# Optimization experiments

Measured on AMD Instinct MI355X. Metric: run time of the kernel, lower is better.

## Reference

```python
import jax, jax.numpy as jnp
import numpy as np

N_NODES = 100000
N_EDGES = 3200000
NFEAT = 256
NHID = 256
NCLASS = 64


def setup_inputs() -> dict:
    key = jax.random.key(0)
    ks = jax.random.split(key, 12)
    x = jax.random.normal(ks[0], (N_NODES, NFEAT), dtype=jnp.float32)
    edge_src = jax.random.randint(ks[1], (N_EDGES,), 0, N_NODES, dtype=jnp.int32)
    edge_dst = jnp.sort(jax.random.randint(ks[2], (N_EDGES,), 0, N_NODES, dtype=jnp.int32))
    edge_w = jax.random.uniform(ks[3], (N_EDGES,), dtype=jnp.float32)
    s1 = 1.0 / np.sqrt(NFEAT)
    s2 = 1.0 / np.sqrt(NHID)
    W1 = jax.random.normal(ks[4], (NFEAT, NHID), dtype=jnp.float32) * s1
    b1 = jnp.zeros((NHID,), dtype=jnp.float32)
    W2 = jax.random.normal(ks[5], (NHID, NHID), dtype=jnp.float32) * s2
    b2 = jnp.zeros((NHID,), dtype=jnp.float32)
    WL1 = jax.random.normal(ks[6], (NHID, NCLASS), dtype=jnp.float32) * s2
    bL1 = jnp.zeros((NCLASS,), dtype=jnp.float32)
    WL2 = jax.random.normal(ks[7], (NHID, NCLASS), dtype=jnp.float32) * s2
    bL2 = jnp.zeros((NCLASS,), dtype=jnp.float32)
    return {"x": x, "edge_src": edge_src, "edge_dst": edge_dst, "edge_w": edge_w,
            "W1": W1, "b1": b1, "W2": W2, "b2": b2,
            "WL1": WL1, "bL1": bL1, "WL2": WL2, "bL2": bL2}


def reference(x, edge_src, edge_dst, edge_w, W1, b1, W2, b2, WL1, bL1, WL2, bL2):
    n = x.shape[0]

    def spmm(h):
        # adj @ h with adj given as (src, dst, w) edge list:
        # out[dst] += w * h[src]
        return jax.ops.segment_sum(edge_w[:, None] * h[edge_src], edge_dst, num_segments=n)

    # GraphConvolution layer 1: support = x @ W; out = adj @ support + b; relu
    # (dropout inactive in eval mode)
    h = jax.nn.relu(spmm(x @ W1) + b1)
    # GraphConvolution layer 2
    h = jax.nn.relu(spmm(h @ W2) + b2)
    # twin dense heads
    logit1 = h @ WL1 + bL1
    logit2 = h @ WL2 + bL2
    return (logit1, logit2)
```

## Files before the change

kernel.cpp:

```cpp
#include <hip/hip_runtime.h>
#include <hip/hip_bf16.h>

typedef __attribute__((ext_vector_type(8))) short short8;
typedef __attribute__((ext_vector_type(4))) float f32x4;
typedef __attribute__((ext_vector_type(2))) float f32x2;

__device__ inline unsigned short f2bf(float f) {
    union { float f; unsigned int u; } x; x.f = f;
    return (unsigned short)((x.u + 0x7fffu + ((x.u >> 16) & 1u)) >> 16);
}

#define ASYNC16(gptr, lptr)                                                      \
    __builtin_amdgcn_global_load_lds(                                            \
        (const __attribute__((address_space(1))) unsigned int*)(gptr),           \
        (__attribute__((address_space(3))) unsigned int*)(lptr), 16, 0, 0)

__device__ __host__ inline int sg(int j) {
    int p = j & 63;
    return (j & ~63) | ((p >> 2) + 16 * (p & 3));
}

__global__ void rowptr_kernel(const int* __restrict__ dst, int* __restrict__ rp,
                              int E, int N) {
    int e = blockIdx.x * blockDim.x + threadIdx.x;
    if (e >= E) return;
    int d1 = dst[e];
    int d0 = (e == 0) ? -1 : dst[e - 1];
    for (int n = d0 + 1; n <= d1; n++) rp[n] = e;
    if (e <= N) {
        int dlast = dst[E - 1];
        if (e > dlast) rp[e] = E;
    }
}

__global__ void epack_kernel(const int* __restrict__ src, const float* __restrict__ w,
                             unsigned int* __restrict__ ep, int E4) {
    int i = blockIdx.x * blockDim.x + threadIdx.x;
    if (i >= E4) return;
    const int4 sv = ((const int4*)src)[i];
    const float4 wv = ((const float4*)w)[i];
    uint4 o;
    o.x = ((unsigned int)(f2bf(wv.x) & 0x7fffu) << 17) | (unsigned int)sv.x;
    o.y = ((unsigned int)(f2bf(wv.y) & 0x7fffu) << 17) | (unsigned int)sv.y;
    o.z = ((unsigned int)(f2bf(wv.z) & 0x7fffu) << 17) | (unsigned int)sv.z;
    o.w = ((unsigned int)(f2bf(wv.w) & 0x7fffu) << 17) | (unsigned int)sv.w;
    ((uint4*)ep)[i] = o;
}

__device__ inline float unpackw(unsigned int p) {
    return __uint_as_float((p >> 17) << 16);
}

__global__ void x2bf_kernel(const float* __restrict__ x, unsigned short* __restrict__ xb,
                            int n8) {
    int i = blockIdx.x * blockDim.x + threadIdx.x;
    if (i >= n8) return;
    const uint4* p = (const uint4*)(x + (size_t)i * 8);
    uint4 u = p[0], v = p[1];
    uint4 pk;
    pk.x = ((u.x + 0x8000u) >> 16) | ((u.y + 0x8000u) & 0xffff0000u);
    pk.y = ((u.z + 0x8000u) >> 16) | ((u.w + 0x8000u) & 0xffff0000u);
    pk.z = ((v.x + 0x8000u) >> 16) | ((v.y + 0x8000u) & 0xffff0000u);
    pk.w = ((v.z + 0x8000u) >> 16) | ((v.w + 0x8000u) & 0xffff0000u);
    *(uint4*)(xb + (size_t)i * 8) = pk;
}

__global__ void prep_kernel(const float* __restrict__ W1, const float* __restrict__ W2,
                            const float* __restrict__ WL1, const float* __restrict__ WL2,
                            const float* __restrict__ b1, const float* __restrict__ b2,
                            unsigned short* __restrict__ W1t, unsigned short* __restrict__ W2t,
                            unsigned short* __restrict__ WLt,
                            float* __restrict__ b1p, float* __restrict__ b2p) {
    int b = blockIdx.x, k = threadIdx.x;
    if (b < 256) {
        W1t[(size_t)b * 256 + k] = f2bf(W1[(size_t)k * 256 + b]);
    } else if (b < 512) {
        int n = b - 256;
        W2t[(size_t)n * 256 + k] = f2bf(W2[(size_t)sg(k) * 256 + n]);
    } else if (b < 640) {
        int c = b - 512;
        int ks = sg(k);
        float v = (c < 64) ? WL1[(size_t)ks * 64 + c] : WL2[(size_t)ks * 64 + (c - 64)];
        WLt[(size_t)c * 256 + k] = f2bf(v);
    } else if (b == 640) {
        b1p[k] = b1[sg(k)];
    } else {
        b2p[k] = b2[sg(k)];
    }
}

__global__ __launch_bounds__(256) void gemm_f8_kernel(
    const unsigned short* __restrict__ A, const unsigned short* __restrict__ Bt,
    unsigned char* __restrict__ C, int M)
{
    __shared__ __align__(16) unsigned short As[128 * 32];
    __shared__ __align__(16) unsigned short Bs[128 * 32];
    const int t = threadIdx.x;
    const int row0 = blockIdx.y * 128;
    const int col0 = blockIdx.x * 128;
    const int wid = t >> 6, lane = t & 63;
    const int wm = (wid >> 1) * 64, wn = (wid & 1) * 64;
    const int qk = (lane >> 4) * 8, r16 = lane & 15;

    const int c0 = t, c1 = t + 256;
    const int am0 = min(row0 + (c0 >> 2), M - 1);
    const int am1 = min(row0 + (c1 >> 2), M - 1);
    const int ak0 = (c0 & 3) * 8, ak1 = (c1 & 3) * 8;
    const int bm0 = col0 + (c0 >> 2), bm1 = col0 + (c1 >> 2);

    f32x4 acc[4][4];
#pragma unroll
    for (int i = 0; i < 4; i++)
#pragma unroll
        for (int j = 0; j < 4; j++) acc[i][j] = (f32x4){0.f, 0.f, 0.f, 0.f};

    for (int k0 = 0; k0 < 256; k0 += 32) {
        ASYNC16(A + (size_t)am0 * 256 + k0 + ak0, &As[c0 * 8]);
        ASYNC16(A + (size_t)am1 * 256 + k0 + ak1, &As[c1 * 8]);
        ASYNC16(Bt + (size_t)bm0 * 256 + k0 + ak0, &Bs[c0 * 8]);
        ASYNC16(Bt + (size_t)bm1 * 256 + k0 + ak1, &Bs[c1 * 8]);
        __syncthreads();
        short8 av[4], bv[4];
#pragma unroll
        for (int mt = 0; mt < 4; mt++) av[mt] = *(const short8*)(&As[(wm + mt * 16 + r16) * 32 + qk]);
#pragma unroll
        for (int nt = 0; nt < 4; nt++) bv[nt] = *(const short8*)(&Bs[(wn + nt * 16 + r16) * 32 + qk]);
#pragma unroll
        for (int mt = 0; mt < 4; mt++)
#pragma unroll
            for (int nt = 0; nt < 4; nt++)
                acc[mt][nt] = __builtin_amdgcn_mfma_f32_16x16x32_bf16(av[mt], bv[nt], acc[mt][nt], 0, 0, 0);
        __syncthreads();
    }
#pragma unroll
    for (int mt = 0; mt < 4; mt++) {
        const int rowb = row0 + wm + mt * 16 + (lane >> 4) * 4;
#pragma unroll
        for (int r = 0; r < 4; r++) {
            const int row = rowb + r;
            if (row >= M) continue;
            int w = 0;
            w = __builtin_amdgcn_cvt_pk_fp8_f32(acc[mt][0][r], acc[mt][1][r], w, false);
            w = __builtin_amdgcn_cvt_pk_fp8_f32(acc[mt][2][r], acc[mt][3][r], w, true);
            *(unsigned int*)(C + (size_t)row * 256 + col0 + wn + r16 * 4) = (unsigned int)w;
        }
    }
}

__global__ __launch_bounds__(256) void head_kernel(
    const unsigned short* __restrict__ A, const unsigned short* __restrict__ Bt,
    const float* __restrict__ bL1, const float* __restrict__ bL2,
    float* __restrict__ out, int M)
{
    __shared__ __align__(16) unsigned short As[128 * 32];
    __shared__ __align__(16) unsigned short Bs[128 * 32];
    const int t = threadIdx.x;
    const int row0 = blockIdx.x * 128;
    const int wid = t >> 6, lane = t & 63;
    const int wm = (wid >> 1) * 64, wn = (wid & 1) * 64;
    const int qk = (lane >> 4) * 8, r16 = lane & 15;

    const int c0 = t, c1 = t + 256;
    const int am0 = min(row0 + (c0 >> 2), M - 1);
    const int am1 = min(row0 + (c1 >> 2), M - 1);
    const int ak0 = (c0 & 3) * 8, ak1 = (c1 & 3) * 8;
    const int bm0 = c0 >> 2, bm1 = c1 >> 2;

    f32x4 acc[4][4];
#pragma unroll
    for (int i = 0; i < 4; i++)
#pragma unroll
        for (int j = 0; j < 4; j++) acc[i][j] = (f32x4){0.f, 0.f, 0.f, 0.f};

    for (int k0 = 0; k0 < 256; k0 += 32) {
        ASYNC16(A + (size_t)am0 * 256 + k0 + ak0, &As[c0 * 8]);
        ASYNC16(A + (size_t)am1 * 256 + k0 + ak1, &As[c1 * 8]);
        ASYNC16(Bt + (size_t)bm0 * 256 + k0 + ak0, &Bs[c0 * 8]);
        ASYNC16(Bt + (size_t)bm1 * 256 + k0 + ak1, &Bs[c1 * 8]);
        __syncthreads();
        short8 av[4], bv[4];
#pragma unroll
        for (int mt = 0; mt < 4; mt++) av[mt] = *(const short8*)(&As[(wm + mt * 16 + r16) * 32 + qk]);
#pragma unroll
        for (int nt = 0; nt < 4; nt++) bv[nt] = *(const short8*)(&Bs[(wn + nt * 16 + r16) * 32 + qk]);
#pragma unroll
        for (int mt = 0; mt < 4; mt++)
#pragma unroll
            for (int nt = 0; nt < 4; nt++)
                acc[mt][nt] = __builtin_amdgcn_mfma_f32_16x16x32_bf16(av[mt], bv[nt], acc[mt][nt], 0, 0, 0);
        __syncthreads();
    }
#pragma unroll
    for (int mt = 0; mt < 4; mt++) {
#pragma unroll
        for (int r = 0; r < 4; r++) {
            int row = row0 + wm + mt * 16 + (lane >> 4) * 4 + r;
            if (row >= M) continue;
#pragma unroll
            for (int nt = 0; nt < 4; nt++) {
                int col = wn + nt * 16 + r16;
                float v = acc[mt][nt][r];
                if (col < 64) {
                    out[(size_t)row * 64 + col] = v + bL1[col];
                } else {
                    out[(size_t)M * 64 + (size_t)row * 64 + (col - 64)] = v + bL2[col - 64];
                }
            }
        }
    }
}

__device__ inline void acc16f8(float* a, uint4 r, float w) {
    f32x2 p;
    p = __builtin_amdgcn_cvt_pk_f32_fp8((int)r.x, false); a[0]  += w * p.x; a[1]  += w * p.y;
    p = __builtin_amdgcn_cvt_pk_f32_fp8((int)r.x, true);  a[2]  += w * p.x; a[3]  += w * p.y;
    p = __builtin_amdgcn_cvt_pk_f32_fp8((int)r.y, false); a[4]  += w * p.x; a[5]  += w * p.y;
    p = __builtin_amdgcn_cvt_pk_f32_fp8((int)r.y, true);  a[6]  += w * p.x; a[7]  += w * p.y;
    p = __builtin_amdgcn_cvt_pk_f32_fp8((int)r.z, false); a[8]  += w * p.x; a[9]  += w * p.y;
    p = __builtin_amdgcn_cvt_pk_f32_fp8((int)r.z, true);  a[10] += w * p.x; a[11] += w * p.y;
    p = __builtin_amdgcn_cvt_pk_f32_fp8((int)r.w, false); a[12] += w * p.x; a[13] += w * p.y;
    p = __builtin_amdgcn_cvt_pk_f32_fp8((int)r.w, true);  a[14] += w * p.x; a[15] += w * p.y;
}

__global__ __launch_bounds__(256) void spmm_fp8_kernel(
    const unsigned char* __restrict__ sup, const int* __restrict__ rp,
    const unsigned int* __restrict__ ep, const float* __restrict__ bias,
    unsigned short* __restrict__ out, int nnodes)
{
    const int wid = threadIdx.x >> 6, lane = threadIdx.x & 63;
    const int node = blockIdx.x * 4 + wid;
    if (node >= nnodes) return;
    const int g = lane >> 4;
    const int f16 = (lane & 15) * 16;
    const unsigned char* supf = sup + f16;
    const int beg = rp[node], end = rp[node + 1];

    float a[16];
#pragma unroll
    for (int i = 0; i < 16; i++) a[i] = 0.f;

    int e = beg;
    const int nmain = (end - beg) >> 3;
    if (nmain > 0) {
        unsigned int cp0 = ep[e + g], cp1 = ep[e + 4 + g];
        uint4 cr0 = *(const uint4*)(supf + (size_t)(cp0 & 0x1ffffu) * 256);
        uint4 cr1 = *(const uint4*)(supf + (size_t)(cp1 & 0x1ffffu) * 256);
        unsigned int np0 = 0, np1 = 0;
        if (nmain > 1) {
            np0 = ep[e + 8 + g]; np1 = ep[e + 12 + g];
        }
        for (int it = 0; it + 1 < nmain; ++it) {
            const uint4 nr0 = *(const uint4*)(supf + (size_t)(np0 & 0x1ffffu) * 256);
            const uint4 nr1 = *(const uint4*)(supf + (size_t)(np1 & 0x1ffffu) * 256);
            unsigned int mp0 = 0, mp1 = 0;
            if (it + 2 < nmain) {
                const int eb = e + (it + 2) * 8;
                mp0 = ep[eb + g]; mp1 = ep[eb + 4 + g];
            }
            acc16f8(a, cr0, unpackw(cp0));
            acc16f8(a, cr1, unpackw(cp1));
            cr0 = nr0; cr1 = nr1; cp0 = np0; cp1 = np1;
            np0 = mp0; np1 = mp1;
        }
        acc16f8(a, cr0, unpackw(cp0));
        acc16f8(a, cr1, unpackw(cp1));
        e += nmain * 8;
    }
    for (; e + 4 <= end; e += 4) {
        const unsigned int p = ep[e + g];
        const uint4 r = *(const uint4*)(supf + (size_t)(p & 0x1ffffu) * 256);
        acc16f8(a, r, unpackw(p));
    }
    {
        const int rem = end - e;
        if (g < rem) {
            const unsigned int p = ep[e + g];
            const uint4 r = *(const uint4*)(supf + (size_t)(p & 0x1ffffu) * 256);
            acc16f8(a, r, unpackw(p));
        }
    }
#pragma unroll
    for (int i = 0; i < 16; i++) {
        a[i] += __shfl_xor(a[i], 16);
        a[i] += __shfl_xor(a[i], 32);
    }

    if (g == 0) {
        const float4 b0 = *(const float4*)(bias + f16);
        const float4 b1 = *(const float4*)(bias + f16 + 4);
        const float4 b2 = *(const float4*)(bias + f16 + 8);
        const float4 b3 = *(const float4*)(bias + f16 + 12);
        a[0] += b0.x; a[1] += b0.y; a[2]  += b0.z; a[3]  += b0.w;
        a[4] += b1.x; a[5] += b1.y; a[6]  += b1.z; a[7]  += b1.w;
        a[8] += b2.x; a[9] += b2.y; a[10] += b2.z; a[11] += b2.w;
        a[12] += b3.x; a[13] += b3.y; a[14] += b3.z; a[15] += b3.w;
#pragma unroll
        for (int i = 0; i < 16; i++) a[i] = a[i] > 0.f ? a[i] : 0.f;
        uint4 o0, o1;
        o0.x = (unsigned int)f2bf(a[0])  | ((unsigned int)f2bf(a[1])  << 16);
        o0.y = (unsigned int)f2bf(a[2])  | ((unsigned int)f2bf(a[3])  << 16);
        o0.z = (unsigned int)f2bf(a[4])  | ((unsigned int)f2bf(a[5])  << 16);
        o0.w = (unsigned int)f2bf(a[6])  | ((unsigned int)f2bf(a[7])  << 16);
        o1.x = (unsigned int)f2bf(a[8])  | ((unsigned int)f2bf(a[9])  << 16);
        o1.y = (unsigned int)f2bf(a[10]) | ((unsigned int)f2bf(a[11]) << 16);
        o1.z = (unsigned int)f2bf(a[12]) | ((unsigned int)f2bf(a[13]) << 16);
        o1.w = (unsigned int)f2bf(a[14]) | ((unsigned int)f2bf(a[15]) << 16);
        *(uint4*)(out + (size_t)node * 256 + f16) = o0;
        *(uint4*)(out + (size_t)node * 256 + f16 + 8) = o1;
    }
}

__global__ __launch_bounds__(256) void spmm_fp8_raw_kernel(
    const unsigned char* __restrict__ sup, const int* __restrict__ rp,
    const int* __restrict__ esrc, const float* __restrict__ ew,
    const float* __restrict__ bias, unsigned short* __restrict__ out, int nnodes)
{
    const int wid = threadIdx.x >> 6, lane = threadIdx.x & 63;
    const int node = blockIdx.x * 4 + wid;
    if (node >= nnodes) return;
    const int g = lane >> 4;
    const int f16 = (lane & 15) * 16;
    const unsigned char* supf = sup + f16;
    const int beg = rp[node], end = rp[node + 1];

    float a[16];
#pragma unroll
    for (int i = 0; i < 16; i++) a[i] = 0.f;

    int e = beg;
    for (; e + 8 <= end; e += 8) {
        const int s0 = esrc[e + g],     s1 = esrc[e + 4 + g];
        const float w0 = ew[e + g],     w1 = ew[e + 4 + g];
        const uint4 r0 = *(const uint4*)(supf + (size_t)s0 * 256);
        const uint4 r1 = *(const uint4*)(supf + (size_t)s1 * 256);
        acc16f8(a, r0, w0);
        acc16f8(a, r1, w1);
    }
    for (; e + 4 <= end; e += 4) {
        const int s = esrc[e + g];
        const float w = ew[e + g];
        const uint4 r = *(const uint4*)(supf + (size_t)s * 256);
        acc16f8(a, r, w);
    }
    {
        const int rem = end - e;
        if (g < rem) {
            const int s = esrc[e + g];
            const float w = ew[e + g];
            const uint4 r = *(const uint4*)(supf + (size_t)s * 256);
            acc16f8(a, r, w);
        }
    }
#pragma unroll
    for (int i = 0; i < 16; i++) {
        a[i] += __shfl_xor(a[i], 16);
        a[i] += __shfl_xor(a[i], 32);
    }

    if (g == 0) {
        const float4 b0 = *(const float4*)(bias + f16);
        const float4 b1 = *(const float4*)(bias + f16 + 4);
        const float4 b2 = *(const float4*)(bias + f16 + 8);
        const float4 b3 = *(const float4*)(bias + f16 + 12);
        a[0] += b0.x; a[1] += b0.y; a[2]  += b0.z; a[3]  += b0.w;
        a[4] += b1.x; a[5] += b1.y; a[6]  += b1.z; a[7]  += b1.w;
        a[8] += b2.x; a[9] += b2.y; a[10] += b2.z; a[11] += b2.w;
        a[12] += b3.x; a[13] += b3.y; a[14] += b3.z; a[15] += b3.w;
#pragma unroll
        for (int i = 0; i < 16; i++) a[i] = a[i] > 0.f ? a[i] : 0.f;
        uint4 o0, o1;
        o0.x = (unsigned int)f2bf(a[0])  | ((unsigned int)f2bf(a[1])  << 16);
        o0.y = (unsigned int)f2bf(a[2])  | ((unsigned int)f2bf(a[3])  << 16);
        o0.z = (unsigned int)f2bf(a[4])  | ((unsigned int)f2bf(a[5])  << 16);
        o0.w = (unsigned int)f2bf(a[6])  | ((unsigned int)f2bf(a[7])  << 16);
        o1.x = (unsigned int)f2bf(a[8])  | ((unsigned int)f2bf(a[9])  << 16);
        o1.y = (unsigned int)f2bf(a[10]) | ((unsigned int)f2bf(a[11]) << 16);
        o1.z = (unsigned int)f2bf(a[12]) | ((unsigned int)f2bf(a[13]) << 16);
        o1.w = (unsigned int)f2bf(a[14]) | ((unsigned int)f2bf(a[15]) << 16);
        *(uint4*)(out + (size_t)node * 256 + f16) = o0;
        *(uint4*)(out + (size_t)node * 256 + f16 + 8) = o1;
    }
}

extern "C" void kernel_launch(void* const* d_in, const int* in_sizes, int n_in,
                              void* d_out, int out_size, void* d_ws, size_t ws_size,
                              hipStream_t stream) {
    const float* x    = (const float*)d_in[0];
    const int*   esrc = (const int*)d_in[1];
    const int*   edst = (const int*)d_in[2];
    const float* ew   = (const float*)d_in[3];
    const float* W1   = (const float*)d_in[4];
    const float* b1   = (const float*)d_in[5];
    const float* W2   = (const float*)d_in[6];
    const float* b2   = (const float*)d_in[7];
    const float* WL1  = (const float*)d_in[8];
    const float* bL1  = (const float*)d_in[9];
    const float* WL2  = (const float*)d_in[10];
    const float* bL2  = (const float*)d_in[11];
    float* out = (float*)d_out;

    const int N = in_sizes[0] / 256;
    const int E = in_sizes[1];

    char* ws = (char*)d_ws;
    size_t off = 0;
    auto alloc = [&](size_t bytes) -> void* {
        void* p = ws + off;
        off = (off + bytes + 511) & ~(size_t)511;
        return p;
    };
    int* rp              = (int*)alloc((size_t)(N + 1) * 4);
    unsigned short* W1t  = (unsigned short*)alloc((size_t)256 * 256 * 2);
    unsigned short* W2t  = (unsigned short*)alloc((size_t)256 * 256 * 2);
    unsigned short* WLt  = (unsigned short*)alloc((size_t)128 * 256 * 2);
    float* b1p           = (float*)alloc(256 * 4);
    float* b2p           = (float*)alloc(256 * 4);
    unsigned char* sup8  = (unsigned char*)alloc((size_t)N * 256);
    unsigned short* hbuf = (unsigned short*)alloc((size_t)N * 256 * 2);
    unsigned int* ep     = (unsigned int*)alloc((size_t)E * 4);
    const bool packed = (off <= ws_size);

    const int mblocks = (N + 127) / 128;

    rowptr_kernel<<<(E + 255) / 256, 256, 0, stream>>>(edst, rp, E, N);
    if (packed)
        epack_kernel<<<(E / 4 + 255) / 256, 256, 0, stream>>>(esrc, ew, ep, E / 4);
    x2bf_kernel<<<(N * 256 / 8 + 255) / 256, 256, 0, stream>>>(x, hbuf, N * 256 / 8);
    prep_kernel<<<642, 256, 0, stream>>>(W1, W2, WL1, WL2, b1, b2, W1t, W2t, WLt, b1p, b2p);

    gemm_f8_kernel<<<dim3(2, mblocks), 256, 0, stream>>>(hbuf, W1t, sup8, N);
    if (packed)
        spmm_fp8_kernel<<<(N + 3) / 4, 256, 0, stream>>>(sup8, rp, ep, b1p, hbuf, N);
    else
        spmm_fp8_raw_kernel<<<(N + 3) / 4, 256, 0, stream>>>(sup8, rp, esrc, ew, b1p, hbuf, N);
    gemm_f8_kernel<<<dim3(2, mblocks), 256, 0, stream>>>(hbuf, W2t, sup8, N);
    if (packed)
        spmm_fp8_kernel<<<(N + 3) / 4, 256, 0, stream>>>(sup8, rp, ep, b2p, hbuf, N);
    else
        spmm_fp8_raw_kernel<<<(N + 3) / 4, 256, 0, stream>>>(sup8, rp, esrc, ew, b2p, hbuf, N);
    head_kernel<<<mblocks, 256, 0, stream>>>(hbuf, WLt, bL1, bL2, out, N);
}
```

Baseline: 506.2 us.

## Fuse fp32-to-bf16 input conversion into first GEMM and use packed FMA in SpMM

Drops the separate x-to-bf16 conversion kernel and has a new first-layer GEMM read the fp32 input directly, converting each tile to bf16 in registers before storing it to LDS. This removes one full write and re-read of a bf16 copy of x (about 50 MB of traffic) and one kernel launch. Separately, the SpMM accumulation switches to inline-asm v_pk_fma_f32 on float pairs to halve the FMA instruction count. The fused GEMM loads A synchronously instead of through async LDS copies, which may expose more load latency, and because x is fp32 each block reads twice as many A bytes as before.

```diff
diff --git a/kernel.cpp b/kernel.cpp
--- a/kernel.cpp
+++ b/kernel.cpp
@@ -49,20 +49,6 @@
 
 __device__ inline float unpackw(unsigned int p) {
     return __uint_as_float((p >> 17) << 16);
-}
-
-__global__ void x2bf_kernel(const float* __restrict__ x, unsigned short* __restrict__ xb,
-                            int n8) {
-    int i = blockIdx.x * blockDim.x + threadIdx.x;
-    if (i >= n8) return;
-    const uint4* p = (const uint4*)(x + (size_t)i * 8);
-    uint4 u = p[0], v = p[1];
-    uint4 pk;
-    pk.x = ((u.x + 0x8000u) >> 16) | ((u.y + 0x8000u) & 0xffff0000u);
-    pk.y = ((u.z + 0x8000u) >> 16) | ((u.w + 0x8000u) & 0xffff0000u);
-    pk.z = ((v.x + 0x8000u) >> 16) | ((v.y + 0x8000u) & 0xffff0000u);
-    pk.w = ((v.z + 0x8000u) >> 16) | ((v.w + 0x8000u) & 0xffff0000u);
-    *(uint4*)(xb + (size_t)i * 8) = pk;
 }
 
 __global__ void prep_kernel(const float* __restrict__ W1, const float* __restrict__ W2,
@@ -89,6 +75,78 @@
     }
 }
 
+__global__ __launch_bounds__(256) void gemm_f8_x32_kernel(
+    const float* __restrict__ A, const unsigned short* __restrict__ Bt,
+    unsigned char* __restrict__ C, int M)
+{
+    __shared__ __align__(16) unsigned short As[128 * 32];
+    __shared__ __align__(16) unsigned short Bs[128 * 32];
+    const int t = threadIdx.x;
+    const int row0 = blockIdx.y * 128;
+    const int col0 = blockIdx.x * 128;
+    const int wid = t >> 6, lane = t & 63;
+    const int wm = (wid >> 1) * 64, wn = (wid & 1) * 64;
+    const int qk = (lane >> 4) * 8, r16 = lane & 15;
+
+    const int c0 = t, c1 = t + 256;
+    const int am0 = min(row0 + (c0 >> 2), M - 1);
+    const int am1 = min(row0 + (c1 >> 2), M - 1);
+    const int ak0 = (c0 & 3) * 8, ak1 = (c1 & 3) * 8;
+    const int bm0 = col0 + (c0 >> 2), bm1 = col0 + (c1 >> 2);
+
+    f32x4 acc[4][4];
+#pragma unroll
+    for (int i = 0; i < 4; i++)
+#pragma unroll
+        for (int j = 0; j < 4; j++) acc[i][j] = (f32x4){0.f, 0.f, 0.f, 0.f};
+
+    for (int k0 = 0; k0 < 256; k0 += 32) {
+        ASYNC16(Bt + (size_t)bm0 * 256 + k0 + ak0, &Bs[c0 * 8]);
+        ASYNC16(Bt + (size_t)bm1 * 256 + k0 + ak1, &Bs[c1 * 8]);
+        const float* pa0 = A + (size_t)am0 * 256 + k0 + ak0;
+        const float* pa1 = A + (size_t)am1 * 256 + k0 + ak1;
+        const uint4 u0 = *(const uint4*)pa0, v0 = *(const uint4*)(pa0 + 4);
+        const uint4 u1 = *(const uint4*)pa1, v1 = *(const uint4*)(pa1 + 4);
+        uint4 pk0, pk1;
+        pk0.x = ((u0.x + 0x8000u) >> 16) | ((u0.y + 0x8000u) & 0xffff0000u);
+        pk0.y = ((u0.z + 0x8000u) >> 16) | ((u0.w + 0x8000u) & 0xffff0000u);
+        pk0.z = ((v0.x + 0x8000u) >> 16) | ((v0.y + 0x8000u) & 0xffff0000u);
+        pk0.w = ((v0.z + 0x8000u) >> 16) | ((v0.w + 0x8000u) & 0xffff0000u);
+        pk1.x = ((u1.x + 0x8000u) >> 16) | ((u1.y + 0x8000u) & 0xffff0000u);
+        pk1.y = ((u1.z + 0x8000u) >> 16) | ((u1.w + 0x8000u) & 0xffff0000u);
+        pk1.z = ((v1.x + 0x8000u) >> 16) | ((v1.y + 0x8000u) & 0xffff0000u);
+        pk1.w = ((v1.z + 0x8000u) >> 16) | ((v1.w + 0x8000u) & 0xffff0000u);
+        *(uint4*)(&As[c0 * 8]) = pk0;
+        *(uint4*)(&As[c1 * 8]) = pk1;
+        __syncthreads();
+        short8 av[4], bv[4];
+#pragma unroll
+        for (int mt = 0; mt < 4; mt++) av[mt] = *(const short8*)(&As[(wm + mt * 16 + r16) * 32 + qk]);
+#pragma unroll
+        for (int nt = 0; nt < 4; nt++) bv[nt] = *(const short8*)(&Bs[(wn + nt * 16 + r16) * 32 + qk]);
+#pragma unroll
+        for (int mt = 0; mt < 4; mt++)
+#pragma unroll
+            for (int nt = 0; nt < 4; nt++)
+                acc[mt][nt] = __builtin_amdgcn_mfma_f32_16x16x32_bf16(av[mt], bv[nt], acc[mt][nt], 0, 0, 0);
+        __syncthreads();
+    }
+    const int scol0 = col0 + wn + r16 * 4;
+#pragma unroll
+    for (int mt = 0; mt < 4; mt++) {
+        const int rowb = row0 + wm + mt * 16 + (lane >> 4) * 4;
+#pragma unroll
+        for (int r = 0; r < 4; r++) {
+            const int row = rowb + r;
+            if (row >= M) continue;
+            int w = 0;
+            w = __builtin_amdgcn_cvt_pk_fp8_f32(acc[mt][0][r], acc[mt][1][r], w, false);
+            w = __builtin_amdgcn_cvt_pk_fp8_f32(acc[mt][2][r], acc[mt][3][r], w, true);
+            *(unsigned int*)(C + (size_t)row * 256 + scol0) = (unsigned int)w;
+        }
+    }
+}
+
 __global__ __launch_bounds__(256) void gemm_f8_kernel(
     const unsigned short* __restrict__ A, const unsigned short* __restrict__ Bt,
     unsigned char* __restrict__ C, int M)
@@ -210,16 +268,21 @@
     }
 }
 
-__device__ inline void acc16f8(float* a, uint4 r, float w) {
-    f32x2 p;
-    p = __builtin_amdgcn_cvt_pk_f32_fp8((int)r.x, false); a[0]  += w * p.x; a[1]  += w * p.y;
-    p = __builtin_amdgcn_cvt_pk_f32_fp8((int)r.x, true);  a[2]  += w * p.x; a[3]  += w * p.y;
-    p = __builtin_amdgcn_cvt_pk_f32_fp8((int)r.y, false); a[4]  += w * p.x; a[5]  += w * p.y;
-    p = __builtin_amdgcn_cvt_pk_f32_fp8((int)r.y, true);  a[6]  += w * p.x; a[7]  += w * p.y;
-    p = __builtin_amdgcn_cvt_pk_f32_fp8((int)r.z, false); a[8]  += w * p.x; a[9]  += w * p.y;
-    p = __builtin_amdgcn_cvt_pk_f32_fp8((int)r.z, true);  a[10] += w * p.x; a[11] += w * p.y;
-    p = __builtin_amdgcn_cvt_pk_f32_fp8((int)r.w, false); a[12] += w * p.x; a[13] += w * p.y;
-    p = __builtin_amdgcn_cvt_pk_f32_fp8((int)r.w, true);  a[14] += w * p.x; a[15] += w * p.y;
+__device__ inline f32x2 pkfma(f32x2 a, f32x2 b, f32x2 c) {
+    f32x2 d;
+    asm("v_pk_fma_f32 %0, %1, %2, %3" : "=v"(d) : "v"(a), "v"(b), "v"(c));
+    return d;
+}
+
+__device__ inline void acc16f8_pk(f32x2* a2, uint4 r, f32x2 wv) {
+    a2[0] = pkfma(__builtin_amdgcn_cvt_pk_f32_fp8((int)r.x, false), wv, a2[0]);
+    a2[1] = pkfma(__builtin_amdgcn_cvt_pk_f32_fp8((int)r.x, true),  wv, a2[1]);
+    a2[2] = pkfma(__builtin_amdgcn_cvt_pk_f32_fp8((int)r.y, false), wv, a2[2]);
+    a2[3] = pkfma(__builtin_amdgcn_cvt_pk_f32_fp8((int)r.y, true),  wv, a2[3]);
+    a2[4] = pkfma(__builtin_amdgcn_cvt_pk_f32_fp8((int)r.z, false), wv, a2[4]);
+    a2[5] = pkfma(__builtin_amdgcn_cvt_pk_f32_fp8((int)r.z, true),  wv, a2[5]);
+    a2[6] = pkfma(__builtin_amdgcn_cvt_pk_f32_fp8((int)r.w, false), wv, a2[6]);
+    a2[7] = pkfma(__builtin_amdgcn_cvt_pk_f32_fp8((int)r.w, true),  wv, a2[7]);
 }
 
 __global__ __launch_bounds__(256) void spmm_fp8_kernel(
@@ -235,9 +298,9 @@
     const unsigned char* supf = sup + f16;
     const int beg = rp[node], end = rp[node + 1];
 
-    float a[16];
-#pragma unroll
-    for (int i = 0; i < 16; i++) a[i] = 0.f;
+    f32x2 a2[8];
+#pragma unroll
+    for (int i = 0; i < 8; i++) a2[i] = (f32x2){0.f, 0.f};
 
     int e = beg;
     const int nmain = (end - beg) >> 3;
@@ -257,28 +320,36 @@
                 const int eb = e + (it + 2) * 8;
                 mp0 = ep[eb + g]; mp1 = ep[eb + 4 + g];
             }
-            acc16f8(a, cr0, unpackw(cp0));
-            acc16f8(a, cr1, unpackw(cp1));
+            const float w0 = unpackw(cp0), w1 = unpackw(cp1);
+            acc16f8_pk(a2, cr0, (f32x2){w0, w0});
+            acc16f8_pk(a2, cr1, (f32x2){w1, w1});
             cr0 = nr0; cr1 = nr1; cp0 = np0; cp1 = np1;
             np0 = mp0; np1 = mp1;
         }
-        acc16f8(a, cr0, unpackw(cp0));
-        acc16f8(a, cr1, unpackw(cp1));
+        const float w0 = unpackw(cp0), w1 = unpackw(cp1);
+        acc16f8_pk(a2, cr0, (f32x2){w0, w0});
+        acc16f8_pk(a2, cr1, (f32x2){w1, w1});
         e += nmain * 8;
     }
     for (; e + 4 <= end; e += 4) {
         const unsigned int p = ep[e + g];
         const uint4 r = *(const uint4*)(supf + (size_t)(p & 0x1ffffu) * 256);
-        acc16f8(a, r, unpackw(p));
+        const float w = unpackw(p);
+        acc16f8_pk(a2, r, (f32x2){w, w});
     }
     {
         const int rem = end - e;
         if (g < rem) {
             const unsigned int p = ep[e + g];
             const uint4 r = *(const uint4*)(supf + (size_t)(p & 0x1ffffu) * 256);
-            acc16f8(a, r, unpackw(p));
-        }
-    }
+            const float w = unpackw(p);
+            acc16f8_pk(a2, r, (f32x2){w, w});
+        }
+    }
+
+    float a[16];
+#pragma unroll
+    for (int i = 0; i < 8; i++) { a[2 * i] = a2[i].x; a[2 * i + 1] = a2[i].y; }
 #pragma unroll
     for (int i = 0; i < 16; i++) {
         a[i] += __shfl_xor(a[i], 16);
@@ -323,9 +394,9 @@
     const unsigned char* supf = sup + f16;
     const int beg = rp[node], end = rp[node + 1];
 
-    float a[16];
-#pragma unroll
-    for (int i = 0; i < 16; i++) a[i] = 0.f;
+    f32x2 a2[8];
+#pragma unroll
+    for (int i = 0; i < 8; i++) a2[i] = (f32x2){0.f, 0.f};
 
     int e = beg;
     for (; e + 8 <= end; e += 8) {
@@ -333,14 +404,14 @@
         const float w0 = ew[e + g],     w1 = ew[e + 4 + g];
         const uint4 r0 = *(const uint4*)(supf + (size_t)s0 * 256);
         const uint4 r1 = *(const uint4*)(supf + (size_t)s1 * 256);
-        acc16f8(a, r0, w0);
-        acc16f8(a, r1, w1);
+        acc16f8_pk(a2, r0, (f32x2){w0, w0});
+        acc16f8_pk(a2, r1, (f32x2){w1, w1});
     }
     for (; e + 4 <= end; e += 4) {
         const int s = esrc[e + g];
         const float w = ew[e + g];
         const uint4 r = *(const uint4*)(supf + (size_t)s * 256);
-        acc16f8(a, r, w);
+        acc16f8_pk(a2, r, (f32x2){w, w});
     }
     {
         const int rem = end - e;
@@ -348,9 +419,12 @@
             const int s = esrc[e + g];
             const float w = ew[e + g];
             const uint4 r = *(const uint4*)(supf + (size_t)s * 256);
-            acc16f8(a, r, w);
-        }
-    }
+            acc16f8_pk(a2, r, (f32x2){w, w});
+        }
+    }
+    float a[16];
+#pragma unroll
+    for (int i = 0; i < 8; i++) { a[2 * i] = a2[i].x; a[2 * i + 1] = a2[i].y; }
 #pragma unroll
     for (int i = 0; i < 16; i++) {
         a[i] += __shfl_xor(a[i], 16);
@@ -425,10 +499,9 @@
     rowptr_kernel<<<(E + 255) / 256, 256, 0, stream>>>(edst, rp, E, N);
     if (packed)
         epack_kernel<<<(E / 4 + 255) / 256, 256, 0, stream>>>(esrc, ew, ep, E / 4);
-    x2bf_kernel<<<(N * 256 / 8 + 255) / 256, 256, 0, stream>>>(x, hbuf, N * 256 / 8);
     prep_kernel<<<642, 256, 0, stream>>>(W1, W2, WL1, WL2, b1, b2, W1t, W2t, WLt, b1p, b2p);
 
-    gemm_f8_kernel<<<dim3(2, mblocks), 256, 0, stream>>>(hbuf, W1t, sup8, N);
+    gemm_f8_x32_kernel<<<dim3(2, mblocks), 256, 0, stream>>>(x, W1t, sup8, N);
     if (packed)
         spmm_fp8_kernel<<<(N + 3) / 4, 256, 0, stream>>>(sup8, rp, ep, b1p, hbuf, N);
     else
```

Measured after the change: 483.1 us. -4.6%, faster.
